# Performance work log

Measured on AMD Instinct MI355X. Metric: run time of the kernel, lower is better.

The kernel has to match this reference:

```python
import jax, jax.numpy as jnp
import numpy as np

B, L, DM = 1, 512, 768
DS, DC, EX = 64, 4, 2
DI = EX * DM            # d_inner = 1536
DR = DM // 16           # dt_rank = 48


def setup_inputs() -> dict:
    key = jax.random.key(0)
    ks = jax.random.split(key, 12)
    s = 0.02
    inp = {
        "x": jax.random.normal(ks[0], (B, L, DM), dtype=jnp.float32),
        "ln_w": jnp.ones((DM,), jnp.float32),
        "ln_b": jnp.zeros((DM,), jnp.float32),
        "in_proj_w": jax.random.normal(ks[1], (2 * DI, DM), jnp.float32) * s,
        "conv_w": jax.random.normal(ks[2], (DI, 1, DC), jnp.float32) * s,
        "conv_b": jnp.zeros((DI,), jnp.float32),
        "x_proj_w": jax.random.normal(ks[3], (DR + 2 * DS, DI), jnp.float32) * s,
        "dt_proj_w": jax.random.normal(ks[4], (DI, DR), jnp.float32) * s,
        "dt_proj_b": jax.random.normal(ks[5], (DI,), jnp.float32) * s,
        "A_log": jnp.log(jnp.broadcast_to(jnp.arange(1, DS + 1, dtype=jnp.float32), (DI, DS))),
        "D": jnp.ones((DI,), jnp.float32),
        "out_proj_w": jax.random.normal(ks[6], (DM, DI), jnp.float32) * s,
    }
    return inp


def _layernorm(x, w, b, eps=1e-5):
    mu = jnp.mean(x, axis=-1, keepdims=True)
    var = jnp.mean((x - mu) ** 2, axis=-1, keepdims=True)
    return (x - mu) * jax.lax.rsqrt(var + eps) * w + b


def _causal_depthwise_conv(x, w, b):
    # x: [B, L, DI] -> conv over time, depthwise, causal (left pad DC-1)
    xc = jnp.transpose(x, (0, 2, 1))  # [B, DI, L]
    y = jax.lax.conv_general_dilated(
        xc, w, window_strides=(1,), padding=[(DC - 1, 0)],
        dimension_numbers=("NCH", "OIH", "NCH"), feature_group_count=DI)
    y = y + b[None, :, None]
    return jnp.transpose(y, (0, 2, 1))  # [B, L, DI]


def _selective_scan(deltaA, deltaB_u, C):
    # deltaA, deltaB_u: [B, L, DI, DS]; C: [B, L, DS]
    dA = jnp.transpose(deltaA, (1, 0, 2, 3))
    dBu = jnp.transpose(deltaB_u, (1, 0, 2, 3))
    Ct = jnp.transpose(C, (1, 0, 2))
    s0 = jnp.zeros(deltaA.shape[:1] + deltaA.shape[2:], deltaA.dtype).transpose(0, 1, 2)
    s0 = jnp.zeros((deltaA.shape[0], deltaA.shape[2], deltaA.shape[3]), deltaA.dtype)

    def step(s, inp):
        dA_t, dBu_t, C_t = inp
        s = dA_t * s + dBu_t                      # [B, DI, DS]
        y = jnp.einsum("bdn,bn->bd", s, C_t)      # [B, DI]
        return s, y

    _, ys = jax.lax.scan(step, s0, (dA, dBu, Ct))
    return jnp.transpose(ys, (1, 0, 2))           # [B, L, DI]


def reference(x, ln_w, ln_b, in_proj_w, conv_w, conv_b, x_proj_w,
              dt_proj_w, dt_proj_b, A_log, D, out_proj_w):
    residual = x
    h = _layernorm(x, ln_w, ln_b)
    xz = jnp.einsum("bld,ed->ble", h, in_proj_w)  # [B, L, 2*DI]
    x_in, z = jnp.split(xz, 2, axis=-1)
    x_in = jax.nn.silu(_causal_depthwise_conv(x_in, conv_w, conv_b))
    x_dbl = jnp.einsum("bld,ed->ble", x_in, x_proj_w)  # [B, L, DR+2*DS]
    dt, Bm, Cm = jnp.split(x_dbl, [DR, DR + DS], axis=-1)
    dt = jax.nn.softplus(jnp.einsum("blr,dr->bld", dt, dt_proj_w) + dt_proj_b)  # [B,L,DI]
    A = -jnp.exp(A_log)                                 # [DI, DS]
    deltaA = jnp.exp(dt[..., None] * A)                 # [B, L, DI, DS]
    deltaB_u = dt[..., None] * Bm[:, :, None, :] * x_in[..., None]
    y = _selective_scan(deltaA, deltaB_u, Cm)           # [B, L, DI]
    y = y + x_in * D
    y = y * jax.nn.silu(z)
    out = jnp.einsum("bld,ed->ble", y, out_proj_w)      # [B, L, DM]
    return residual + out
```

## Files before the change

### kernel.cpp

```cpp
#include <hip/hip_runtime.h>
#include <hip/hip_bf16.h>
#include <math.h>

#define L_SEQ 512
#define DM 768
#define DI 1536
#define DS 64
#define DC 4
#define DR 48
#define NXD 176
#define NC 8
#define TC 64

typedef __attribute__((ext_vector_type(8))) short short8;
typedef __attribute__((ext_vector_type(4))) float float4v;

#define NWI (2 * DI * DM)
#define NWX (NXD * DI)
#define NWDT (DI * DR)
#define NWO (DM * DI)
#define NXZ (L_SEQ * 2 * DI)
#define NXDBL (L_SEQ * NXD)
#define NXR (L_SEQ * DM)

#define B_LN 512
#define B_WI (NWI / 1024)
#define B_WX (NWX / 1024)
#define B_WDT (NWDT / 1024)
#define B_WO (NWO / 1024)
#define PREP_GRID (B_LN + B_WI + B_WX + B_WDT + B_WO)

__device__ __forceinline__ float bp_add(float p, int addr) {
  return p + __int_as_float(__builtin_amdgcn_ds_bpermute(addr, __float_as_int(p)));
}
__device__ __forceinline__ float lane_read(float v, int t) {
  return __int_as_float(__builtin_amdgcn_readlane(__float_as_int(v), t));
}
__device__ __forceinline__ short f2bf(float v) {
  __hip_bfloat16 h = __float2bfloat16(v);
  return *reinterpret_cast<short*>(&h);
}
__device__ __forceinline__ short8 cvt8f(const float* p, bool valid) {
  float4 u = *(const float4*)(p);
  float4 v = *(const float4*)(p + 4);
  short8 r;
  r[0] = f2bf(u.x); r[1] = f2bf(u.y); r[2] = f2bf(u.z); r[3] = f2bf(u.w);
  r[4] = f2bf(v.x); r[5] = f2bf(v.y); r[6] = f2bf(v.z); r[7] = f2bf(v.w);
  if (!valid) r = (short8)0;
  return r;
}

__device__ __forceinline__ void cvt_blk(const float* __restrict__ s,
                                        short* __restrict__ d, int b) {
  int i = b * 1024 + threadIdx.x * 4;
  float4 v = *(const float4*)(s + i);
  short4 o; o.x = f2bf(v.x); o.y = f2bf(v.y); o.z = f2bf(v.z); o.w = f2bf(v.w);
  *(short4*)(d + i) = o;
}
__global__ __launch_bounds__(256) void prep(
    const float* __restrict__ x, const float* __restrict__ lnw,
    const float* __restrict__ lnb, short* __restrict__ h,
    const float* __restrict__ wi, short* __restrict__ wib,
    const float* __restrict__ wx, short* __restrict__ wxb,
    const float* __restrict__ wdt, short* __restrict__ wdtb,
    const float* __restrict__ wo, short* __restrict__ wob) {
  int b = blockIdx.x;
  if (b < B_LN) {
    int l = b, tid = threadIdx.x;
    const float* xr = x + l * DM;
    float s = 0.f, s2 = 0.f;
    for (int i = tid; i < DM; i += 256) { float t = xr[i]; s += t; s2 += t * t; }
#pragma unroll
    for (int off = 32; off; off >>= 1) { s += __shfl_xor(s, off); s2 += __shfl_xor(s2, off); }
    __shared__ float ls[4], ls2[4];
    int wid = tid >> 6, lane = tid & 63;
    if (lane == 0) { ls[wid] = s; ls2[wid] = s2; }
    __syncthreads();
    s = ls[0] + ls[1] + ls[2] + ls[3];
    s2 = ls2[0] + ls2[1] + ls2[2] + ls2[3];
    float mean = s * (1.f / DM);
    float var = s2 * (1.f / DM) - mean * mean;
    float rstd = rsqrtf(var + 1e-5f);
    for (int i = tid; i < DM; i += 256)
      h[l * DM + i] = f2bf((xr[i] - mean) * rstd * lnw[i] + lnb[i]);
    return;
  }
  b -= B_LN;
  if (b < B_WI) { cvt_blk(wi, wib, b); return; }
  b -= B_WI;
  if (b < B_WX) { cvt_blk(wx, wxb, b); return; }
  b -= B_WX;
  if (b < B_WDT) { cvt_blk(wdt, wdtb, b); return; }
  b -= B_WDT;
  cvt_blk(wo, wob, b);
}

__global__ __launch_bounds__(256) void gemm_bf16(const short* __restrict__ A, int lda,
                                                 const short* __restrict__ B,
                                                 float* __restrict__ C,
                                                 int N, int K,
                                                 const float* __restrict__ res,
                                                 int mode) {
  int lane = threadIdx.x & 63, w = threadIdx.x >> 6;
  int fr = lane & 15, koff = (lane >> 4) * 8;
  int mbase = blockIdx.y * 64 + (w & 1) * 32;
  int nbase = blockIdx.x * 64 + (w >> 1) * 32;
  int kchunk = K / gridDim.z;
  int kbeg = blockIdx.z * kchunk;
  int nr0 = nbase + fr;      if (nr0 > N - 1) nr0 = N - 1;
  int nr1 = nbase + 16 + fr; if (nr1 > N - 1) nr1 = N - 1;
  const short* pA0 = A + (size_t)(mbase + fr) * lda + koff + kbeg;
  const short* pA1 = pA0 + (size_t)16 * lda;
  const short* pB0 = B + (size_t)nr0 * K + koff + kbeg;
  const short* pB1 = B + (size_t)nr1 * K + koff + kbeg;
  float4v acc00 = (float4v){0.f,0.f,0.f,0.f}, acc01 = acc00;
  float4v acc10 = acc00, acc11 = acc00;
  short8 a0A = *(const short8*)(pA0);      short8 a1A = *(const short8*)(pA1);
  short8 b0A = *(const short8*)(pB0);      short8 b1A = *(const short8*)(pB1);
  short8 a0B = *(const short8*)(pA0 + 32); short8 a1B = *(const short8*)(pA1 + 32);
  short8 b0B = *(const short8*)(pB0 + 32); short8 b1B = *(const short8*)(pB1 + 32);
  for (int k0 = 0; k0 < kchunk; k0 += 64) {
    short8 ca0 = a0A, ca1 = a1A, cb0 = b0A, cb1 = b1A;
    short8 da0 = a0B, da1 = a1B, db0 = b0B, db1 = b1B;
    int nA = k0 + 64; if (nA >= kchunk) nA = 0;
    int nB = k0 + 96; if (nB >= kchunk) nB = 32;
    a0A = *(const short8*)(pA0 + nA); a1A = *(const short8*)(pA1 + nA);
    b0A = *(const short8*)(pB0 + nA); b1A = *(const short8*)(pB1 + nA);
    a0B = *(const short8*)(pA0 + nB); a1B = *(const short8*)(pA1 + nB);
    b0B = *(const short8*)(pB0 + nB); b1B = *(const short8*)(pB1 + nB);
    acc00 = __builtin_amdgcn_mfma_f32_16x16x32_bf16(ca0, cb0, acc00, 0, 0, 0);
    acc01 = __builtin_amdgcn_mfma_f32_16x16x32_bf16(ca0, cb1, acc01, 0, 0, 0);
    acc10 = __builtin_amdgcn_mfma_f32_16x16x32_bf16(ca1, cb0, acc10, 0, 0, 0);
    acc11 = __builtin_amdgcn_mfma_f32_16x16x32_bf16(ca1, cb1, acc11, 0, 0, 0);
    acc00 = __builtin_amdgcn_mfma_f32_16x16x32_bf16(da0, db0, acc00, 0, 0, 0);
    acc01 = __builtin_amdgcn_mfma_f32_16x16x32_bf16(da0, db1, acc01, 0, 0, 0);
    acc10 = __builtin_amdgcn_mfma_f32_16x16x32_bf16(da1, db0, acc10, 0, 0, 0);
    acc11 = __builtin_amdgcn_mfma_f32_16x16x32_bf16(da1, db1, acc11, 0, 0, 0);
  }
  float* Cz = C + (size_t)blockIdx.z * (size_t)L_SEQ * (size_t)N;
  int col0 = nbase + fr, col1 = nbase + 16 + fr;
  int rb = mbase + (lane >> 4) * 4;
#pragma unroll
  for (int r = 0; r < 4; ++r) {
    size_t o00 = (size_t)(rb + r) * N;
    size_t o10 = (size_t)(rb + 16 + r) * N;
    if (col0 < N) {
      float v0 = acc00[r], v1 = acc10[r];
      if (mode == 2) { v0 += res[o00 + col0]; v1 += res[o10 + col0]; }
      Cz[o00 + col0] = v0; Cz[o10 + col0] = v1;
    }
    if (col1 < N) {
      float v0 = acc01[r], v1 = acc11[r];
      if (mode == 2) { v0 += res[o00 + col1]; v1 += res[o10 + col1]; }
      Cz[o00 + col1] = v0; Cz[o10 + col1] = v1;
    }
  }
}

__global__ __launch_bounds__(256) void reduce_add(const float* __restrict__ part,
                                                  int MN, int splitk,
                                                  float* __restrict__ out) {
  int i = blockIdx.x * 256 + threadIdx.x;
  if (i >= MN) return;
  float a = 0.f;
  for (int z = 0; z < splitk; ++z) a += part[(size_t)z * MN + i];
  out[i] = a;
}

__global__ __launch_bounds__(256) void dtp_gemm(const float* __restrict__ Axd,
                                                const short* __restrict__ Bw,
                                                float* __restrict__ dt,
                                                const float* __restrict__ bias) {
  int lane = threadIdx.x & 63, w = threadIdx.x >> 6;
  int fr = lane & 15, koff = (lane >> 4) * 8;
  int mbase = blockIdx.y * 64 + (w & 1) * 32;
  int nbase = blockIdx.x * 64 + (w >> 1) * 32;
  const float* pA0 = Axd + (size_t)(mbase + fr) * NXD;
  const float* pA1 = pA0 + (size_t)16 * NXD;
  const short* pB0 = Bw + (size_t)(nbase + fr) * DR;
  const short* pB1 = Bw + (size_t)(nbase + 16 + fr) * DR;
  float4v acc00 = (float4v){0.f,0.f,0.f,0.f}, acc01 = acc00;
  float4v acc10 = acc00, acc11 = acc00;
#pragma unroll
  for (int k0 = 0; k0 < 64; k0 += 32) {
    bool valid = (k0 + koff) < DR;
    int off = valid ? k0 + koff : 0;
    short8 a0 = cvt8f(pA0 + off, valid);
    short8 a1 = cvt8f(pA1 + off, valid);
    short8 b0 = *(const short8*)(pB0 + off);
    short8 b1 = *(const short8*)(pB1 + off);
    if (!valid) { b0 = (short8)0; b1 = (short8)0; }
    acc00 = __builtin_amdgcn_mfma_f32_16x16x32_bf16(a0, b0, acc00, 0, 0, 0);
    acc01 = __builtin_amdgcn_mfma_f32_16x16x32_bf16(a0, b1, acc01, 0, 0, 0);
    acc10 = __builtin_amdgcn_mfma_f32_16x16x32_bf16(a1, b0, acc10, 0, 0, 0);
    acc11 = __builtin_amdgcn_mfma_f32_16x16x32_bf16(a1, b1, acc11, 0, 0, 0);
  }
  int col0 = nbase + fr, col1 = nbase + 16 + fr;
  float bi0 = bias[col0], bi1 = bias[col1];
  int rb = mbase + (lane >> 4) * 4;
#pragma unroll
  for (int r = 0; r < 4; ++r) {
    float v0 = acc00[r] + bi0, v1 = acc01[r] + bi1;
    float v2 = acc10[r] + bi0, v3 = acc11[r] + bi1;
    v0 = (v0 > 20.f) ? v0 : log1pf(__expf(v0));
    v1 = (v1 > 20.f) ? v1 : log1pf(__expf(v1));
    v2 = (v2 > 20.f) ? v2 : log1pf(__expf(v2));
    v3 = (v3 > 20.f) ? v3 : log1pf(__expf(v3));
    dt[(size_t)(rb + r) * DI + col0] = v0;
    dt[(size_t)(rb + r) * DI + col1] = v1;
    dt[(size_t)(rb + 16 + r) * DI + col0] = v2;
    dt[(size_t)(rb + 16 + r) * DI + col1] = v3;
  }
}

__global__ __launch_bounds__(256) void conv_silu_kernel(const float* __restrict__ xz,
                                                        const float* __restrict__ cw,
                                                        const float* __restrict__ cb,
                                                        float* __restrict__ xc,
                                                        short* __restrict__ xcb) {
  int idx = blockIdx.x * 256 + threadIdx.x;
  if (idx >= L_SEQ * DI) return;
  int l = idx / DI, d = idx - l * DI;
  float acc = cb[d];
#pragma unroll
  for (int j = 0; j < DC; ++j) {
    int ll = l - (DC - 1) + j;
    if (ll >= 0) acc = fmaf(xz[(size_t)ll * (2 * DI) + d], cw[d * DC + j], acc);
  }
  float sig = 1.f / (1.f + __expf(-acc));
  float v = acc * sig;
  xc[idx] = v;
  xcb[idx] = f2bf(v);
}

__global__ __launch_bounds__(256) void scan_p1(const float* __restrict__ dt,
                                               const float* __restrict__ xc,
                                               const float* __restrict__ xdbl,
                                               const float* __restrict__ A_log,
                                               float* __restrict__ send,
                                               float* __restrict__ dts) {
  int lane = threadIdx.x & 63;
  int wid = threadIdx.x >> 6;
  int pair = blockIdx.x * 4 + wid;
  int c = __builtin_amdgcn_readfirstlane(pair / DI);
  int d = __builtin_amdgcn_readfirstlane(pair - (pair / DI) * DI);
  float A = -__expf(A_log[(size_t)d * DS + lane]);
  int l0 = c * TC;
  float dtv = dt[(size_t)(l0 + lane) * DI + d];
  float xv  = xc[(size_t)(l0 + lane) * DI + d];
  const float* pB = xdbl + (size_t)l0 * NXD + DR + lane;
  float s = 0.f;
#pragma unroll 8
  for (int t = 0; t < TC; ++t) {
    float dt_c = lane_read(dtv, t);
    float x_c  = lane_read(xv, t);
    float B_c  = pB[(size_t)t * NXD];
    float dA = __expf(dt_c * A);
    s = fmaf(dA, s, dt_c * x_c * B_c);
  }
  float dsum = dtv;
  dsum = bp_add(dsum, (lane ^ 1) << 2);  dsum = bp_add(dsum, (lane ^ 2) << 2);
  dsum = bp_add(dsum, (lane ^ 4) << 2);  dsum = bp_add(dsum, (lane ^ 8) << 2);
  dsum = bp_add(dsum, (lane ^ 16) << 2); dsum = bp_add(dsum, (lane ^ 32) << 2);
  send[((size_t)c * DI + d) * DS + lane] = s;
  if (lane == 0) dts[c * DI + d] = dsum;
}

__global__ __launch_bounds__(256) void scan_p2(const float* __restrict__ send,
                                               const float* __restrict__ dts,
                                               const float* __restrict__ A_log,
                                               float* __restrict__ sinit) {
  int lane = threadIdx.x & 63;
  int wid = threadIdx.x >> 6;
  int d = __builtin_amdgcn_readfirstlane(blockIdx.x * 4 + wid);
  float A = -__expf(A_log[(size_t)d * DS + lane]);
  float s = 0.f;
  for (int c = 1; c < NC; ++c) {
    float P = __expf(A * dts[(c - 1) * DI + d]);
    s = fmaf(P, s, send[((size_t)(c - 1) * DI + d) * DS + lane]);
    sinit[((size_t)c * DI + d) * DS + lane] = s;
  }
}

__global__ __launch_bounds__(256) void scan_p3(const float* __restrict__ dt,
                                               const float* __restrict__ xc,
                                               const float* __restrict__ xdbl,
                                               const float* __restrict__ A_log,
                                               const float* __restrict__ Dv,
                                               const float* __restrict__ xz,
                                               const float* __restrict__ sinit,
                                               short* __restrict__ y) {
  __shared__ float Pb[4][16][66];
  int lane = threadIdx.x & 63;
  int wid = threadIdx.x >> 6;
  int pair = blockIdx.x * 4 + wid;
  int c = __builtin_amdgcn_readfirstlane(pair / DI);
  int d = __builtin_amdgcn_readfirstlane(pair - (pair / DI) * DI);
  float A = -__expf(A_log[(size_t)d * DS + lane]);
  float Dd = Dv[d];
  int l0 = c * TC;
  float dtv = dt[(size_t)(l0 + lane) * DI + d];
  float xv  = xc[(size_t)(l0 + lane) * DI + d];
  float zv  = xz[(size_t)(l0 + lane) * (2 * DI) + DI + d];
  float s = (c == 0) ? 0.f : sinit[((size_t)c * DI + d) * DS + lane];
  const float* pB = xdbl + (size_t)l0 * NXD + DR + lane;
  float yv = 0.f;
#pragma unroll
  for (int sb = 0; sb < 4; ++sb) {
    float P[16];
#pragma unroll
    for (int j = 0; j < 16; ++j) {
      int t = sb * 16 + j;
      float dt_c = lane_read(dtv, t);
      float x_c  = lane_read(xv, t);
      float B_c  = pB[(size_t)t * NXD];
      float C_c  = pB[(size_t)t * NXD + DS];
      float dA = __expf(dt_c * A);
      s = fmaf(dA, s, dt_c * x_c * B_c);
      P[j] = s * C_c;
    }
#pragma unroll
    for (int j = 0; j < 16; ++j) Pb[wid][j][lane] = P[j];
    int t4 = lane >> 2, q = lane & 3;
    const float* row = &Pb[wid][t4][q * 16];
    float part = 0.f;
#pragma unroll
    for (int k = 0; k < 8; ++k) {
      float2 v2 = *(const float2*)(row + 2 * k);
      part += v2.x + v2.y;
    }
    part = bp_add(part, (lane ^ 1) << 2);
    part = bp_add(part, (lane ^ 2) << 2);
    float got = __int_as_float(
        __builtin_amdgcn_ds_bpermute((lane & 15) << 4, __float_as_int(part)));
    yv = ((lane >> 4) == sb) ? got : yv;
  }
  float sig = 1.f / (1.f + __expf(-zv));
  y[(size_t)(l0 + lane) * DI + d] = f2bf((yv + xv * Dd) * (zv * sig));
}

extern "C" void kernel_launch(void* const* d_in, const int* in_sizes, int n_in,
                              void* d_out, int out_size, void* d_ws, size_t ws_size,
                              hipStream_t stream) {
  const float* x         = (const float*)d_in[0];
  const float* ln_w      = (const float*)d_in[1];
  const float* ln_b      = (const float*)d_in[2];
  const float* in_proj_w = (const float*)d_in[3];
  const float* conv_w    = (const float*)d_in[4];
  const float* conv_b    = (const float*)d_in[5];
  const float* x_proj_w  = (const float*)d_in[6];
  const float* dt_proj_w = (const float*)d_in[7];
  const float* dt_proj_b = (const float*)d_in[8];
  const float* A_log     = (const float*)d_in[9];
  const float* Dv        = (const float*)d_in[10];
  const float* out_proj_w= (const float*)d_in[11];
  float* out = (float*)d_out;

  float* ws = (float*)d_ws;
  float* xz    = ws;
  float* xconv = xz + NXZ;
  float* xdbl  = xconv + 786432;
  float* dtb   = xdbl + NXDBL;
  float* send  = dtb + 786432;
  float* dts   = send + 688128;
  float* sinit = dts + 10752;
  float* part2 = sinit + 786432;
  float* fend  = part2 + 720896;
  short* h_bf   = (short*)fend;
  short* wi_bf  = h_bf + NXR;
  short* wx_bf  = wi_bf + NWI;
  short* wdt_bf = wx_bf + NWX;
  short* wo_bf  = wdt_bf + NWDT;
  short* xc_bf  = wo_bf + NWO;
  short* y_bf   = xc_bf + (L_SEQ * DI);

  prep<<<PREP_GRID, 256, 0, stream>>>(x, ln_w, ln_b, h_bf,
                                      in_proj_w, wi_bf, x_proj_w, wx_bf,
                                      dt_proj_w, wdt_bf, out_proj_w, wo_bf);

  gemm_bf16<<<dim3(2 * DI / 64, L_SEQ / 64, 1), 256, 0, stream>>>(
      h_bf, DM, wi_bf, xz, 2 * DI, DM, nullptr, 0);

  conv_silu_kernel<<<(L_SEQ * DI) / 256, 256, 0, stream>>>(xz, conv_w, conv_b,
                                                           xconv, xc_bf);

  gemm_bf16<<<dim3((NXD + 63) / 64, L_SEQ / 64, 8), 256, 0, stream>>>(
      xc_bf, DI, wx_bf, part2, NXD, DI, nullptr, 0);
  reduce_add<<<(NXDBL + 255) / 256, 256, 0, stream>>>(part2, NXDBL, 8, xdbl);

  dtp_gemm<<<dim3(DI / 64, L_SEQ / 64), 256, 0, stream>>>(
      xdbl, wdt_bf, dtb, dt_proj_b);

  scan_p1<<<((NC - 1) * DI) / 4, 256, 0, stream>>>(dtb, xconv, xdbl, A_log, send, dts);
  scan_p2<<<DI / 4, 256, 0, stream>>>(send, dts, A_log, sinit);
  scan_p3<<<(NC * DI) / 4, 256, 0, stream>>>(dtb, xconv, xdbl, A_log, Dv, xz, sinit, y_bf);

  gemm_bf16<<<dim3(DM / 64, L_SEQ / 64, 1), 256, 0, stream>>>(
      y_bf, DI, wo_bf, out, DM, DI, x, 2);
}
```

Before: 212.4 us.

## Fold dt_proj into x_proj weights and use intra-block split-K GEMMs

Precomputes a combined weight (dt_proj_w · x_proj_w[:DR]) inside the prep kernel, so dt comes straight from one GEMM over x_conv alongside the B/C projections. This removes the split-K partial buffer, the reduce kernel and the separate dt GEMM. All GEMMs now use 32x32 tiles with a 4-wave split-K reduced through shared memory, which gives more blocks. scan_p2 is dropped: each scan_p3 chunk recomputes its starting state from chunk-end states. The costs are a per-call 1536x1536x48 weight product plus a much larger x_proj GEMM (1664 outputs instead of 176), and dt now rounds through bf16 weights of the fused product.

```diff
diff --git a/kernel.cpp b/kernel.cpp
--- a/kernel.cpp
+++ b/kernel.cpp
@@ -8,27 +8,20 @@
 #define DS 64
 #define DC 4
 #define DR 48
-#define NXD 176
+#define NBC 128
+#define NP2 (NBC + DI)
 #define NC 8
 #define TC 64
 
 typedef __attribute__((ext_vector_type(8))) short short8;
 typedef __attribute__((ext_vector_type(4))) float float4v;
 
-#define NWI (2 * DI * DM)
-#define NWX (NXD * DI)
-#define NWDT (DI * DR)
-#define NWO (DM * DI)
-#define NXZ (L_SEQ * 2 * DI)
-#define NXDBL (L_SEQ * NXD)
-#define NXR (L_SEQ * DM)
-
-#define B_LN 512
-#define B_WI (NWI / 1024)
-#define B_WX (NWX / 1024)
-#define B_WDT (NWDT / 1024)
-#define B_WO (NWO / 1024)
-#define PREP_GRID (B_LN + B_WI + B_WX + B_WDT + B_WO)
+#define J_LN 512
+#define J_WI (2 * DI * DM / 1024)
+#define J_WBC (NBC * DI / 1024)
+#define J_WO (DM * DI / 1024)
+#define J_WEFF ((DI / 64) * (DI / 64))
+#define PREP_GRID (J_LN + J_WI + J_WBC + J_WO + J_WEFF)
 
 __device__ __forceinline__ float bp_add(float p, int addr) {
   return p + __int_as_float(__builtin_amdgcn_ds_bpermute(addr, __float_as_int(p)));
@@ -49,7 +42,6 @@
   if (!valid) r = (short8)0;
   return r;
 }
-
 __device__ __forceinline__ void cvt_blk(const float* __restrict__ s,
                                         short* __restrict__ d, int b) {
   int i = b * 1024 + threadIdx.x * 4;
@@ -57,73 +49,30 @@
   short4 o; o.x = f2bf(v.x); o.y = f2bf(v.y); o.z = f2bf(v.z); o.w = f2bf(v.w);
   *(short4*)(d + i) = o;
 }
-__global__ __launch_bounds__(256) void prep(
-    const float* __restrict__ x, const float* __restrict__ lnw,
-    const float* __restrict__ lnb, short* __restrict__ h,
-    const float* __restrict__ wi, short* __restrict__ wib,
-    const float* __restrict__ wx, short* __restrict__ wxb,
-    const float* __restrict__ wdt, short* __restrict__ wdtb,
-    const float* __restrict__ wo, short* __restrict__ wob) {
-  int b = blockIdx.x;
-  if (b < B_LN) {
-    int l = b, tid = threadIdx.x;
-    const float* xr = x + l * DM;
-    float s = 0.f, s2 = 0.f;
-    for (int i = tid; i < DM; i += 256) { float t = xr[i]; s += t; s2 += t * t; }
-#pragma unroll
-    for (int off = 32; off; off >>= 1) { s += __shfl_xor(s, off); s2 += __shfl_xor(s2, off); }
-    __shared__ float ls[4], ls2[4];
-    int wid = tid >> 6, lane = tid & 63;
-    if (lane == 0) { ls[wid] = s; ls2[wid] = s2; }
-    __syncthreads();
-    s = ls[0] + ls[1] + ls[2] + ls[3];
-    s2 = ls2[0] + ls2[1] + ls2[2] + ls2[3];
-    float mean = s * (1.f / DM);
-    float var = s2 * (1.f / DM) - mean * mean;
-    float rstd = rsqrtf(var + 1e-5f);
-    for (int i = tid; i < DM; i += 256)
-      h[l * DM + i] = f2bf((xr[i] - mean) * rstd * lnw[i] + lnb[i]);
-    return;
-  }
-  b -= B_LN;
-  if (b < B_WI) { cvt_blk(wi, wib, b); return; }
-  b -= B_WI;
-  if (b < B_WX) { cvt_blk(wx, wxb, b); return; }
-  b -= B_WX;
-  if (b < B_WDT) { cvt_blk(wdt, wdtb, b); return; }
-  b -= B_WDT;
-  cvt_blk(wo, wob, b);
-}
-
-__global__ __launch_bounds__(256) void gemm_bf16(const short* __restrict__ A, int lda,
-                                                 const short* __restrict__ B,
-                                                 float* __restrict__ C,
-                                                 int N, int K,
-                                                 const float* __restrict__ res,
-                                                 int mode) {
-  int lane = threadIdx.x & 63, w = threadIdx.x >> 6;
+
+__device__ __forceinline__ float4v gemm32_core(
+    const short* __restrict__ A, int lda, const short* __restrict__ B, int ldb,
+    int K, int bx, int by, int lane, int w, float4v* red,
+    int* prow, int* pcol) {
+  int ks = K >> 2;
+  int kbeg = w * ks;
   int fr = lane & 15, koff = (lane >> 4) * 8;
-  int mbase = blockIdx.y * 64 + (w & 1) * 32;
-  int nbase = blockIdx.x * 64 + (w >> 1) * 32;
-  int kchunk = K / gridDim.z;
-  int kbeg = blockIdx.z * kchunk;
-  int nr0 = nbase + fr;      if (nr0 > N - 1) nr0 = N - 1;
-  int nr1 = nbase + 16 + fr; if (nr1 > N - 1) nr1 = N - 1;
-  const short* pA0 = A + (size_t)(mbase + fr) * lda + koff + kbeg;
+  int m0 = by * 32, n0 = bx * 32;
+  const short* pA0 = A + (size_t)(m0 + fr) * lda + koff + kbeg;
   const short* pA1 = pA0 + (size_t)16 * lda;
-  const short* pB0 = B + (size_t)nr0 * K + koff + kbeg;
-  const short* pB1 = B + (size_t)nr1 * K + koff + kbeg;
+  const short* pB0 = B + (size_t)(n0 + fr) * ldb + koff + kbeg;
+  const short* pB1 = pB0 + (size_t)16 * ldb;
   float4v acc00 = (float4v){0.f,0.f,0.f,0.f}, acc01 = acc00;
   float4v acc10 = acc00, acc11 = acc00;
   short8 a0A = *(const short8*)(pA0);      short8 a1A = *(const short8*)(pA1);
   short8 b0A = *(const short8*)(pB0);      short8 b1A = *(const short8*)(pB1);
   short8 a0B = *(const short8*)(pA0 + 32); short8 a1B = *(const short8*)(pA1 + 32);
   short8 b0B = *(const short8*)(pB0 + 32); short8 b1B = *(const short8*)(pB1 + 32);
-  for (int k0 = 0; k0 < kchunk; k0 += 64) {
+  for (int k0 = 0; k0 < ks; k0 += 64) {
     short8 ca0 = a0A, ca1 = a1A, cb0 = b0A, cb1 = b1A;
     short8 da0 = a0B, da1 = a1B, db0 = b0B, db1 = b1B;
-    int nA = k0 + 64; if (nA >= kchunk) nA = 0;
-    int nB = k0 + 96; if (nB >= kchunk) nB = 32;
+    int nA = k0 + 64; if (nA >= ks) nA = 0;
+    int nB = k0 + 96; if (nB >= ks) nB = 32;
     a0A = *(const short8*)(pA0 + nA); a1A = *(const short8*)(pA1 + nA);
     b0A = *(const short8*)(pB0 + nA); b1A = *(const short8*)(pB1 + nA);
     a0B = *(const short8*)(pA0 + nB); a1B = *(const short8*)(pA1 + nB);
@@ -137,80 +86,104 @@
     acc10 = __builtin_amdgcn_mfma_f32_16x16x32_bf16(da1, db0, acc10, 0, 0, 0);
     acc11 = __builtin_amdgcn_mfma_f32_16x16x32_bf16(da1, db1, acc11, 0, 0, 0);
   }
-  float* Cz = C + (size_t)blockIdx.z * (size_t)L_SEQ * (size_t)N;
-  int col0 = nbase + fr, col1 = nbase + 16 + fr;
-  int rb = mbase + (lane >> 4) * 4;
-#pragma unroll
-  for (int r = 0; r < 4; ++r) {
-    size_t o00 = (size_t)(rb + r) * N;
-    size_t o10 = (size_t)(rb + 16 + r) * N;
-    if (col0 < N) {
-      float v0 = acc00[r], v1 = acc10[r];
-      if (mode == 2) { v0 += res[o00 + col0]; v1 += res[o10 + col0]; }
-      Cz[o00 + col0] = v0; Cz[o10 + col0] = v1;
-    }
-    if (col1 < N) {
-      float v0 = acc01[r], v1 = acc11[r];
-      if (mode == 2) { v0 += res[o00 + col1]; v1 += res[o10 + col1]; }
-      Cz[o00 + col1] = v0; Cz[o10 + col1] = v1;
-    }
-  }
-}
-
-__global__ __launch_bounds__(256) void reduce_add(const float* __restrict__ part,
-                                                  int MN, int splitk,
-                                                  float* __restrict__ out) {
-  int i = blockIdx.x * 256 + threadIdx.x;
-  if (i >= MN) return;
-  float a = 0.f;
-  for (int z = 0; z < splitk; ++z) a += part[(size_t)z * MN + i];
-  out[i] = a;
-}
-
-__global__ __launch_bounds__(256) void dtp_gemm(const float* __restrict__ Axd,
-                                                const short* __restrict__ Bw,
-                                                float* __restrict__ dt,
-                                                const float* __restrict__ bias) {
+  red[(w * 4 + 0) * 64 + lane] = acc00;
+  red[(w * 4 + 1) * 64 + lane] = acc01;
+  red[(w * 4 + 2) * 64 + lane] = acc10;
+  red[(w * 4 + 3) * 64 + lane] = acc11;
+  __syncthreads();
+  float4v v = red[(0 * 4 + w) * 64 + lane];
+  v = v + red[(1 * 4 + w) * 64 + lane];
+  v = v + red[(2 * 4 + w) * 64 + lane];
+  v = v + red[(3 * 4 + w) * 64 + lane];
+  int qi = w & 1, qj = w >> 1;
+  *prow = m0 + qi * 16 + (lane >> 4) * 4;
+  *pcol = n0 + qj * 16 + (lane & 15);
+  return v;
+}
+
+__global__ __launch_bounds__(256) void prep(
+    const float* __restrict__ x, const float* __restrict__ lnw,
+    const float* __restrict__ lnb, short* __restrict__ h,
+    const float* __restrict__ wi, short* __restrict__ wib,
+    const float* __restrict__ wx, const float* __restrict__ wdt,
+    short* __restrict__ wcomb, const float* __restrict__ wo,
+    short* __restrict__ wob) {
+  __shared__ float ls[4], ls2[4];
+  int b = blockIdx.x;
+  int tid = threadIdx.x, lane = tid & 63, w = tid >> 6;
+  if (b < J_LN) {
+    int l = b;
+    const float* xr = x + l * DM;
+    float s = 0.f, s2 = 0.f;
+    for (int i = tid; i < DM; i += 256) { float t = xr[i]; s += t; s2 += t * t; }
+#pragma unroll
+    for (int off = 32; off; off >>= 1) { s += __shfl_xor(s, off); s2 += __shfl_xor(s2, off); }
+    if (lane == 0) { ls[w] = s; ls2[w] = s2; }
+    __syncthreads();
+    s = ls[0] + ls[1] + ls[2] + ls[3];
+    s2 = ls2[0] + ls2[1] + ls2[2] + ls2[3];
+    float mean = s * (1.f / DM);
+    float var = s2 * (1.f / DM) - mean * mean;
+    float rstd = rsqrtf(var + 1e-5f);
+    for (int i = tid; i < DM; i += 256)
+      h[l * DM + i] = f2bf((xr[i] - mean) * rstd * lnw[i] + lnb[i]);
+    return;
+  }
+  b -= J_LN;
+  if (b < J_WI) { cvt_blk(wi, wib, b); return; }
+  b -= J_WI;
+  if (b < J_WBC) { cvt_blk(wx + DR * DI, wcomb, b); return; }
+  b -= J_WBC;
+  if (b < J_WO) { cvt_blk(wo, wob, b); return; }
+  b -= J_WO;
+  {
+    int tm = b / (DI / 64), tn = b % (DI / 64);
+    int qi = w & 1, qj = w >> 1;
+    int m0 = tm * 64 + qi * 32, n0 = tn * 64 + qj * 32;
+    int fr = lane & 15, koff = (lane >> 4) * 8;
+    const float* pA0 = wdt + (size_t)(m0 + fr) * DR;
+    const float* pA1 = pA0 + (size_t)16 * DR;
+    float4v a00 = (float4v){0.f,0.f,0.f,0.f}, a01 = a00, a10 = a00, a11 = a00;
+#pragma unroll
+    for (int k0 = 0; k0 < 64; k0 += 32) {
+      bool valid = (k0 + koff) < DR;
+      int off = valid ? k0 + koff : 0;
+      short8 fa0 = cvt8f(pA0 + off, valid);
+      short8 fa1 = cvt8f(pA1 + off, valid);
+      short8 fb0, fb1;
+#pragma unroll
+      for (int j = 0; j < 8; ++j) {
+        int r = k0 + koff + j;
+        fb0[j] = valid ? f2bf(wx[(size_t)r * DI + n0 + fr]) : (short)0;
+        fb1[j] = valid ? f2bf(wx[(size_t)r * DI + n0 + 16 + fr]) : (short)0;
+      }
+      a00 = __builtin_amdgcn_mfma_f32_16x16x32_bf16(fa0, fb0, a00, 0, 0, 0);
+      a01 = __builtin_amdgcn_mfma_f32_16x16x32_bf16(fa0, fb1, a01, 0, 0, 0);
+      a10 = __builtin_amdgcn_mfma_f32_16x16x32_bf16(fa1, fb0, a10, 0, 0, 0);
+      a11 = __builtin_amdgcn_mfma_f32_16x16x32_bf16(fa1, fb1, a11, 0, 0, 0);
+    }
+    int rb = (lane >> 4) * 4, cb = lane & 15;
+#pragma unroll
+    for (int r = 0; r < 4; ++r) {
+      wcomb[(size_t)(NBC + m0 + rb + r) * DI + n0 + cb]      = f2bf(a00[r]);
+      wcomb[(size_t)(NBC + m0 + rb + r) * DI + n0 + 16 + cb] = f2bf(a01[r]);
+      wcomb[(size_t)(NBC + m0 + 16 + rb + r) * DI + n0 + cb]      = f2bf(a10[r]);
+      wcomb[(size_t)(NBC + m0 + 16 + rb + r) * DI + n0 + 16 + cb] = f2bf(a11[r]);
+    }
+  }
+}
+
+__global__ __launch_bounds__(256) void k_inproj(const short* __restrict__ h,
+                                                const short* __restrict__ wi,
+                                                float* __restrict__ xz) {
+  __shared__ float4v red[16 * 64];
   int lane = threadIdx.x & 63, w = threadIdx.x >> 6;
-  int fr = lane & 15, koff = (lane >> 4) * 8;
-  int mbase = blockIdx.y * 64 + (w & 1) * 32;
-  int nbase = blockIdx.x * 64 + (w >> 1) * 32;
-  const float* pA0 = Axd + (size_t)(mbase + fr) * NXD;
-  const float* pA1 = pA0 + (size_t)16 * NXD;
-  const short* pB0 = Bw + (size_t)(nbase + fr) * DR;
-  const short* pB1 = Bw + (size_t)(nbase + 16 + fr) * DR;
-  float4v acc00 = (float4v){0.f,0.f,0.f,0.f}, acc01 = acc00;
-  float4v acc10 = acc00, acc11 = acc00;
-#pragma unroll
-  for (int k0 = 0; k0 < 64; k0 += 32) {
-    bool valid = (k0 + koff) < DR;
-    int off = valid ? k0 + koff : 0;
-    short8 a0 = cvt8f(pA0 + off, valid);
-    short8 a1 = cvt8f(pA1 + off, valid);
-    short8 b0 = *(const short8*)(pB0 + off);
-    short8 b1 = *(const short8*)(pB1 + off);
-    if (!valid) { b0 = (short8)0; b1 = (short8)0; }
-    acc00 = __builtin_amdgcn_mfma_f32_16x16x32_bf16(a0, b0, acc00, 0, 0, 0);
-    acc01 = __builtin_amdgcn_mfma_f32_16x16x32_bf16(a0, b1, acc01, 0, 0, 0);
-    acc10 = __builtin_amdgcn_mfma_f32_16x16x32_bf16(a1, b0, acc10, 0, 0, 0);
-    acc11 = __builtin_amdgcn_mfma_f32_16x16x32_bf16(a1, b1, acc11, 0, 0, 0);
-  }
-  int col0 = nbase + fr, col1 = nbase + 16 + fr;
-  float bi0 = bias[col0], bi1 = bias[col1];
-  int rb = mbase + (lane >> 4) * 4;
-#pragma unroll
-  for (int r = 0; r < 4; ++r) {
-    float v0 = acc00[r] + bi0, v1 = acc01[r] + bi1;
-    float v2 = acc10[r] + bi0, v3 = acc11[r] + bi1;
-    v0 = (v0 > 20.f) ? v0 : log1pf(__expf(v0));
-    v1 = (v1 > 20.f) ? v1 : log1pf(__expf(v1));
-    v2 = (v2 > 20.f) ? v2 : log1pf(__expf(v2));
-    v3 = (v3 > 20.f) ? v3 : log1pf(__expf(v3));
-    dt[(size_t)(rb + r) * DI + col0] = v0;
-    dt[(size_t)(rb + r) * DI + col1] = v1;
-    dt[(size_t)(rb + 16 + r) * DI + col0] = v2;
-    dt[(size_t)(rb + 16 + r) * DI + col1] = v3;
-  }
+  int row, col;
+  float4v v = gemm32_core(h, DM, wi, DM, DM, blockIdx.x, blockIdx.y,
+                          lane, w, red, &row, &col);
+#pragma unroll
+  for (int r = 0; r < 4; ++r)
+    xz[(size_t)(row + r) * (2 * DI) + col] = v[r];
 }
 
 __global__ __launch_bounds__(256) void conv_silu_kernel(const float* __restrict__ xz,
@@ -219,7 +192,6 @@
                                                         float* __restrict__ xc,
                                                         short* __restrict__ xcb) {
   int idx = blockIdx.x * 256 + threadIdx.x;
-  if (idx >= L_SEQ * DI) return;
   int l = idx / DI, d = idx - l * DI;
   float acc = cb[d];
 #pragma unroll
@@ -233,9 +205,35 @@
   xcb[idx] = f2bf(v);
 }
 
+__global__ __launch_bounds__(256) void k_proj2(const short* __restrict__ xc,
+                                               const short* __restrict__ wcomb,
+                                               float* __restrict__ xdblBC,
+                                               float* __restrict__ dtb,
+                                               const float* __restrict__ bias) {
+  __shared__ float4v red[16 * 64];
+  int lane = threadIdx.x & 63, w = threadIdx.x >> 6;
+  int row, col;
+  float4v v = gemm32_core(xc, DI, wcomb, DI, DI, blockIdx.x, blockIdx.y,
+                          lane, w, red, &row, &col);
+  if (col < NBC) {
+#pragma unroll
+    for (int r = 0; r < 4; ++r)
+      xdblBC[(size_t)(row + r) * NBC + col] = v[r];
+  } else {
+    int d = col - NBC;
+    float bi = bias[d];
+#pragma unroll
+    for (int r = 0; r < 4; ++r) {
+      float t = v[r] + bi;
+      t = (t > 20.f) ? t : log1pf(__expf(t));
+      dtb[(size_t)(row + r) * DI + d] = t;
+    }
+  }
+}
+
 __global__ __launch_bounds__(256) void scan_p1(const float* __restrict__ dt,
                                                const float* __restrict__ xc,
-                                               const float* __restrict__ xdbl,
+                                               const float* __restrict__ xdblBC,
                                                const float* __restrict__ A_log,
                                                float* __restrict__ send,
                                                float* __restrict__ dts) {
@@ -248,13 +246,13 @@
   int l0 = c * TC;
   float dtv = dt[(size_t)(l0 + lane) * DI + d];
   float xv  = xc[(size_t)(l0 + lane) * DI + d];
-  const float* pB = xdbl + (size_t)l0 * NXD + DR + lane;
+  const float* pB = xdblBC + (size_t)l0 * NBC + lane;
   float s = 0.f;
 #pragma unroll 8
   for (int t = 0; t < TC; ++t) {
     float dt_c = lane_read(dtv, t);
     float x_c  = lane_read(xv, t);
-    float B_c  = pB[(size_t)t * NXD];
+    float B_c  = pB[(size_t)t * NBC];
     float dA = __expf(dt_c * A);
     s = fmaf(dA, s, dt_c * x_c * B_c);
   }
@@ -266,29 +264,14 @@
   if (lane == 0) dts[c * DI + d] = dsum;
 }
 
-__global__ __launch_bounds__(256) void scan_p2(const float* __restrict__ send,
-                                               const float* __restrict__ dts,
-                                               const float* __restrict__ A_log,
-                                               float* __restrict__ sinit) {
-  int lane = threadIdx.x & 63;
-  int wid = threadIdx.x >> 6;
-  int d = __builtin_amdgcn_readfirstlane(blockIdx.x * 4 + wid);
-  float A = -__expf(A_log[(size_t)d * DS + lane]);
-  float s = 0.f;
-  for (int c = 1; c < NC; ++c) {
-    float P = __expf(A * dts[(c - 1) * DI + d]);
-    s = fmaf(P, s, send[((size_t)(c - 1) * DI + d) * DS + lane]);
-    sinit[((size_t)c * DI + d) * DS + lane] = s;
-  }
-}
-
 __global__ __launch_bounds__(256) void scan_p3(const float* __restrict__ dt,
                                                const float* __restrict__ xc,
-                                               const float* __restrict__ xdbl,
+                                               const float* __restrict__ xdblBC,
                                                const float* __restrict__ A_log,
                                                const float* __restrict__ Dv,
                                                const float* __restrict__ xz,
-                                               const float* __restrict__ sinit,
+                                               const float* __restrict__ send,
+                                               const float* __restrict__ dts,
                                                short* __restrict__ y) {
   __shared__ float Pb[4][16][66];
   int lane = threadIdx.x & 63;
@@ -302,8 +285,12 @@
   float dtv = dt[(size_t)(l0 + lane) * DI + d];
   float xv  = xc[(size_t)(l0 + lane) * DI + d];
   float zv  = xz[(size_t)(l0 + lane) * (2 * DI) + DI + d];
-  float s = (c == 0) ? 0.f : sinit[((size_t)c * DI + d) * DS + lane];
-  const float* pB = xdbl + (size_t)l0 * NXD + DR + lane;
+  float s = 0.f;
+  for (int cc = 0; cc < c; ++cc) {
+    float P = __expf(A * dts[cc * DI + d]);
+    s = fmaf(P, s, send[((size_t)cc * DI + d) * DS + lane]);
+  }
+  const float* pB = xdblBC + (size_t)l0 * NBC + lane;
   float yv = 0.f;
 #pragma unroll
   for (int sb = 0; sb < 4; ++sb) {
@@ -313,8 +300,8 @@
       int t = sb * 16 + j;
       float dt_c = lane_read(dtv, t);
       float x_c  = lane_read(xv, t);
-      float B_c  = pB[(size_t)t * NXD];
-      float C_c  = pB[(size_t)t * NXD + DS];
+      float B_c  = pB[(size_t)t * NBC];
+      float C_c  = pB[(size_t)t * NBC + DS];
       float dA = __expf(dt_c * A);
       s = fmaf(dA, s, dt_c * x_c * B_c);
       P[j] = s * C_c;
@@ -337,6 +324,20 @@
   }
   float sig = 1.f / (1.f + __expf(-zv));
   y[(size_t)(l0 + lane) * DI + d] = f2bf((yv + xv * Dd) * (zv * sig));
+}
+
+__global__ __launch_bounds__(256) void k_outproj(const short* __restrict__ y,
+                                                 const short* __restrict__ wo,
+                                                 const float* __restrict__ x,
+                                                 float* __restrict__ out) {
+  __shared__ float4v red[16 * 64];
+  int lane = threadIdx.x & 63, w = threadIdx.x >> 6;
+  int row, col;
+  float4v v = gemm32_core(y, DI, wo, DI, DI, blockIdx.x, blockIdx.y,
+                          lane, w, red, &row, &col);
+#pragma unroll
+  for (int r = 0; r < 4; ++r)
+    out[(size_t)(row + r) * DM + col] = v[r] + x[(size_t)(row + r) * DM + col];
 }
 
 extern "C" void kernel_launch(void* const* d_in, const int* in_sizes, int n_in,
@@ -357,44 +358,36 @@
   float* out = (float*)d_out;
 
   float* ws = (float*)d_ws;
-  float* xz    = ws;
-  float* xconv = xz + NXZ;
-  float* xdbl  = xconv + 786432;
-  float* dtb   = xdbl + NXDBL;
-  float* send  = dtb + 786432;
-  float* dts   = send + 688128;
-  float* sinit = dts + 10752;
-  float* part2 = sinit + 786432;
-  float* fend  = part2 + 720896;
+  float* xz     = ws;
+  float* xconv  = xz + 1572864;
+  float* xdblBC = xconv + 786432;
+  float* dtb    = xdblBC + 65536;
+  float* send   = dtb + 786432;
+  float* dts    = send + 688128;
+  float* fend   = dts + 10752;
   short* h_bf   = (short*)fend;
-  short* wi_bf  = h_bf + NXR;
-  short* wx_bf  = wi_bf + NWI;
-  short* wdt_bf = wx_bf + NWX;
-  short* wo_bf  = wdt_bf + NWDT;
-  short* xc_bf  = wo_bf + NWO;
-  short* y_bf   = xc_bf + (L_SEQ * DI);
-
-  prep<<<PREP_GRID, 256, 0, stream>>>(x, ln_w, ln_b, h_bf,
-                                      in_proj_w, wi_bf, x_proj_w, wx_bf,
-                                      dt_proj_w, wdt_bf, out_proj_w, wo_bf);
-
-  gemm_bf16<<<dim3(2 * DI / 64, L_SEQ / 64, 1), 256, 0, stream>>>(
-      h_bf, DM, wi_bf, xz, 2 * DI, DM, nullptr, 0);
+  short* wi_bf  = h_bf + 393216;
+  short* wo_bf  = wi_bf + 2359296;
+  short* wcomb  = wo_bf + 1179648;
+  short* xc_bf  = wcomb + 2555904;
+  short* y_bf   = xc_bf + 786432;
+
+  prep<<<PREP_GRID, 256, 0, stream>>>(x, ln_w, ln_b, h_bf, in_proj_w, wi_bf,
+                                      x_proj_w, dt_proj_w, wcomb,
+                                      out_proj_w, wo_bf);
+
+  k_inproj<<<dim3(2 * DI / 32, L_SEQ / 32), 256, 0, stream>>>(h_bf, wi_bf, xz);
 
   conv_silu_kernel<<<(L_SEQ * DI) / 256, 256, 0, stream>>>(xz, conv_w, conv_b,
                                                            xconv, xc_bf);
 
-  gemm_bf16<<<dim3((NXD + 63) / 64, L_SEQ / 64, 8), 256, 0, stream>>>(
-      xc_bf, DI, wx_bf, part2, NXD, DI, nullptr, 0);
-  reduce_add<<<(NXDBL + 255) / 256, 256, 0, stream>>>(part2, NXDBL, 8, xdbl);
-
-  dtp_gemm<<<dim3(DI / 64, L_SEQ / 64), 256, 0, stream>>>(
-      xdbl, wdt_bf, dtb, dt_proj_b);
-
-  scan_p1<<<((NC - 1) * DI) / 4, 256, 0, stream>>>(dtb, xconv, xdbl, A_log, send, dts);
-  scan_p2<<<DI / 4, 256, 0, stream>>>(send, dts, A_log, sinit);
-  scan_p3<<<(NC * DI) / 4, 256, 0, stream>>>(dtb, xconv, xdbl, A_log, Dv, xz, sinit, y_bf);
-
-  gemm_bf16<<<dim3(DM / 64, L_SEQ / 64, 1), 256, 0, stream>>>(
-      y_bf, DI, wo_bf, out, DM, DI, x, 2);
-}
+  k_proj2<<<dim3(NP2 / 32, L_SEQ / 32), 256, 0, stream>>>(
+      xc_bf, wcomb, xdblBC, dtb, dt_proj_b);
+
+  scan_p1<<<((NC - 1) * DI) / 4, 256, 0, stream>>>(dtb, xconv, xdblBC, A_log,
+                                                   send, dts);
+  scan_p3<<<(NC * DI) / 4, 256, 0, stream>>>(dtb, xconv, xdblBC, A_log, Dv, xz,
+                                             send, dts, y_bf);
+
+  k_outproj<<<dim3(DM / 32, L_SEQ / 32), 256, 0, stream>>>(y_bf, wo_bf, x, out);
+}
```

New measurement: 205.0 us. -3.5%, faster.
